# Optimization experiments

Hardware: AMD Instinct MI355X
Metric: run time of the kernel (lower is better)

## Reference

```python
import jax, jax.numpy as jnp
import numpy as np

BETA = 0.25

def conv1d(x, w, b=None, stride=1, pad=0):
    # x: (B, C_in, T), w: (C_out, C_in, K)
    y = jax.lax.conv_general_dilated(x, w, (stride,), [(pad, pad)],
                                     dimension_numbers=('NCW', 'OIW', 'NCW'))
    if b is not None:
        y = y + b[None, :, None]
    return y

def setup_inputs() -> dict:
    key = jax.random.key(0)
    ks = jax.random.split(key, 16)
    B, C_in, T = 64, 64, 4096
    h, rh, D, K = 128, 64, 64, 512
    s = 0.05
    f32 = jnp.float32
    return {
        'x': jax.random.normal(ks[0], (B, C_in, T), f32),
        'w1': jax.random.normal(ks[1], (h // 2, C_in, 4), f32) * s,
        'b1': jnp.zeros((h // 2,), f32),
        'w2': jax.random.normal(ks[2], (h, h // 2, 4), f32) * s,
        'b2': jnp.zeros((h,), f32),
        'w3': jax.random.normal(ks[3], (h, h, 3), f32) * s,
        'b3': jnp.zeros((h,), f32),
        'res0_w1': jax.random.normal(ks[4], (rh, h, 3), f32) * s,
        'res0_w2': jax.random.normal(ks[5], (h, rh, 1), f32) * s,
        'res1_w1': jax.random.normal(ks[6], (rh, h, 3), f32) * s,
        'res1_w2': jax.random.normal(ks[7], (h, rh, 1), f32) * s,
        'w_out': jax.random.normal(ks[8], (D, h, 1), f32) * s,
        'b_out': jnp.zeros((D,), f32),
        'wpq': jax.random.normal(ks[9], (D, D, 1), f32) * s,
        'bpq': jnp.zeros((D,), f32),
        'codebook': jax.random.uniform(ks[10], (K, D), f32, -1.0 / K, 1.0 / K),
    }

def reference(x, w1, b1, w2, b2, w3, b3, res0_w1, res0_w2, res1_w1, res1_w2,
              w_out, b_out, wpq, bpq, codebook):
    # ---- Encoder (1D conv downsampling + residual stack) ----
    hcur = jax.nn.relu(conv1d(x, w1, b1, stride=2, pad=1))       # (B, h/2, T/2)
    hcur = jax.nn.relu(conv1d(hcur, w2, b2, stride=2, pad=1))    # (B, h, T/4)
    hcur = conv1d(hcur, w3, b3, stride=1, pad=1)                 # (B, h, T')
    for wa, wb in ((res0_w1, res0_w2), (res1_w1, res1_w2)):
        hcur = hcur + conv1d(jax.nn.relu(conv1d(jax.nn.relu(hcur), wa, None, 1, 1)), wb, None, 1, 0)
    hcur = jax.nn.relu(hcur)
    hcur = conv1d(hcur, w_out, b_out)                            # (B, D, T')
    # ---- pre-quantization 1x1 conv (module permutes to channel-first and back) ----
    z = conv1d(hcur, wpq, bpq)                                   # (B, D, T')
    z_e = jnp.transpose(z, (0, 2, 1))                            # (B, T', D)
    B, Tq, D = z_e.shape
    K = codebook.shape[0]
    # ---- Vector quantization ----
    flat = z_e.reshape(-1, D)                                    # (N, D)
    d = (jnp.sum(flat * flat, axis=1, keepdims=True)
         + jnp.sum(codebook * codebook, axis=1)[None, :]
         - 2.0 * flat @ codebook.T)                              # (N, K)
    idx = jnp.argmin(d, axis=1)                                  # (N,)
    encodings = jax.nn.one_hot(idx, K, dtype=z_e.dtype)          # (N, K)
    z_q = codebook[idx].reshape(B, Tq, D)                        # gather
    sg = jax.lax.stop_gradient
    embedding_loss = jnp.mean((sg(z_q) - z_e) ** 2) + BETA * jnp.mean((z_q - sg(z_e)) ** 2)
    z_q_st = z_e + sg(z_q - z_e)                                 # straight-through
    e_mean = jnp.mean(encodings, axis=0)
    perplexity = jnp.exp(-jnp.sum(e_mean * jnp.log(e_mean + 1e-10)))
    encoding_indices = idx.reshape(-1, 1)
    return (embedding_loss, z_q_st, perplexity, z_e, encodings, encoding_indices)
```

## Files before the change

### kernel.cpp

```cpp
#include <hip/hip_runtime.h>
#include <math.h>


typedef short short8 __attribute__((ext_vector_type(8)));
typedef float f32x4 __attribute__((ext_vector_type(4)));

__device__ __forceinline__ unsigned short bf16hi(float f) {
  unsigned u = __builtin_bit_cast(unsigned, f);
  return (unsigned short)((u + 0x7FFFu + ((u >> 16) & 1u)) >> 16);
}
__device__ __forceinline__ float bf16tof(unsigned short h) {
  unsigned u = ((unsigned)h) << 16;
  return __builtin_bit_cast(float, u);
}
__device__ __forceinline__ void split3(float f, unsigned short& h,
                                       unsigned short& m, unsigned short& l) {
  h = bf16hi(f);
  float r = f - bf16tof(h);
  m = bf16hi(r);
  l = bf16hi(r - bf16tof(m));
}

template<int CIN, int TAPS, int S, bool RELU_IN, bool HAS_BIAS, bool RESID,
         bool CHW_IN, bool OUT_NOGUARD>
__global__ __launch_bounds__(256) void conv_mfma(
    const float* __restrict__ in, const short* __restrict__ Ab,
    const float* __restrict__ bias, const float* __restrict__ resid,
    float* __restrict__ out, int Tin, int Tout, int MTG)
{
  constexpr int nCk   = CIN / 32;
  constexpr int RS    = (S == 2) ? 130 : ((TAPS == 3) ? 66 : 64);
  constexpr int ROWBS = 40;

  __shared__ short xhi[RS * ROWBS];
  __shared__ short xmd[RS * ROWBS];
  __shared__ short xlo[RS * ROWBS];

  const int tid  = threadIdx.x;
  const int lane = tid & 63;
  const int wv   = tid >> 6;
  const int ih   = wv & 1;
  const int jh   = wv >> 1;
  const int tl   = lane & 15;
  const int q    = lane >> 4;
  const int b    = blockIdx.y;
  const int t0   = blockIdx.x * 64;
  const int co0  = blockIdx.z * 64;
  const int COUT = MTG * 16;

  const int rbase = (S == 2) ? (2 * t0) : ((TAPS == 3) ? t0 : (t0 + 1));

  f32x4 acc[2][2] = {};

  for (int ch = 0; ch < nCk; ch++) {
    if (ch) __syncthreads();

    if constexpr (!CHW_IN) {
      for (int i = tid; i < RS * 8; i += 256) {
        int rl = i >> 3;
        int c4 = (i & 7) * 4;
        int rg = rbase + rl;
        const float* sp = in + ((size_t)b * (Tin + 2) + rg) * CIN + ch * 32 + c4;
        float4 v = *(const float4*)sp;
        if (RELU_IN) {
          v.x = fmaxf(v.x, 0.f); v.y = fmaxf(v.y, 0.f);
          v.z = fmaxf(v.z, 0.f); v.w = fmaxf(v.w, 0.f);
        }
        float vv[4] = {v.x, v.y, v.z, v.w};
        unsigned short h[4], m[4], l[4];
        #pragma unroll
        for (int e = 0; e < 4; e++) split3(vv[e], h[e], m[e], l[e]);
        int slot = (S == 2) ? ((rl & 1) * 65 + (rl >> 1)) : rl;
        int off = slot * ROWBS + c4;
        uint2 uh, um, ul;
        uh.x = (unsigned)h[0] | ((unsigned)h[1] << 16);
        uh.y = (unsigned)h[2] | ((unsigned)h[3] << 16);
        um.x = (unsigned)m[0] | ((unsigned)m[1] << 16);
        um.y = (unsigned)m[2] | ((unsigned)m[3] << 16);
        ul.x = (unsigned)l[0] | ((unsigned)l[1] << 16);
        ul.y = (unsigned)l[2] | ((unsigned)l[3] << 16);
        *(uint2*)(xhi + off) = uh;
        *(uint2*)(xmd + off) = um;
        *(uint2*)(xlo + off) = ul;
      }
    } else {
      if (tid < 32) {
        int cig = ch * 32 + tid;
        int tin = 2 * t0 - 1;
        float v = 0.f;
        if (tin >= 0) v = in[((size_t)b * 64 + cig) * Tin + tin];
        unsigned short h, m, l;
        split3(v, h, m, l);
        xhi[tid] = (short)h;
        xmd[tid] = (short)m;
        xlo[tid] = (short)l;
      }
      int cil = tid >> 3, tq = tid & 7;
      for (int base = tq * 4; base <= 128; base += 32) {
        int tin0 = 2 * t0 + base;
        const float* sp = in + ((size_t)b * 64 + ch * 32 + cil) * Tin + tin0;
        float vv[4];
        if (tin0 + 3 < Tin) {
          float4 t4 = *(const float4*)sp;
          vv[0] = t4.x; vv[1] = t4.y; vv[2] = t4.z; vv[3] = t4.w;
        } else {
          #pragma unroll
          for (int e = 0; e < 4; e++) vv[e] = (tin0 + e < Tin) ? sp[e] : 0.f;
        }
        #pragma unroll
        for (int e = 0; e < 4; e++) {
          int rl = base + e + 1;
          if (rl <= 129) {
            unsigned short h, m, l;
            split3(vv[e], h, m, l);
            int slot = (rl & 1) * 65 + (rl >> 1);
            xhi[slot * ROWBS + cil] = (short)h;
            xmd[slot * ROWBS + cil] = (short)m;
            xlo[slot * ROWBS + cil] = (short)l;
          }
        }
      }
    }
    __syncthreads();

    #pragma unroll
    for (int tap = 0; tap < TAPS; tap++) {
      short8 ah[2], am[2], al[2];
      #pragma unroll
      for (int mi = 0; mi < 2; mi++) {
        const short* ab = Ab +
            (size_t)(((ch * TAPS + tap) * MTG + (co0 >> 4) + ih * 2 + mi) * 3) * 512
            + lane * 8;
        ah[mi] = *(const short8*)ab;
        am[mi] = *(const short8*)(ab + 512);
        al[mi] = *(const short8*)(ab + 1024);
      }
      #pragma unroll
      for (int nt = 0; nt < 2; nt++) {
        int tpos = jh * 32 + nt * 16 + tl;
        int slot;
        if constexpr (S == 2)         slot = (tap & 1) * 65 + tpos + (tap >> 1);
        else if constexpr (TAPS == 3) slot = tpos + tap;
        else                          slot = tpos;
        const int xo = slot * ROWBS + q * 8;
        short8 bh = *(const short8*)(xhi + xo);
        short8 bm = *(const short8*)(xmd + xo);
        short8 bl = *(const short8*)(xlo + xo);
        #pragma unroll
        for (int mi = 0; mi < 2; mi++) {
          acc[mi][nt] = __builtin_amdgcn_mfma_f32_16x16x32_bf16(ah[mi], bh, acc[mi][nt], 0, 0, 0);
          acc[mi][nt] = __builtin_amdgcn_mfma_f32_16x16x32_bf16(ah[mi], bm, acc[mi][nt], 0, 0, 0);
          acc[mi][nt] = __builtin_amdgcn_mfma_f32_16x16x32_bf16(am[mi], bh, acc[mi][nt], 0, 0, 0);
          acc[mi][nt] = __builtin_amdgcn_mfma_f32_16x16x32_bf16(am[mi], bm, acc[mi][nt], 0, 0, 0);
          acc[mi][nt] = __builtin_amdgcn_mfma_f32_16x16x32_bf16(ah[mi], bl, acc[mi][nt], 0, 0, 0);
          acc[mi][nt] = __builtin_amdgcn_mfma_f32_16x16x32_bf16(al[mi], bh, acc[mi][nt], 0, 0, 0);
        }
      }
    }
  }

  #pragma unroll
  for (int mi = 0; mi < 2; mi++) {
    #pragma unroll
    for (int nt = 0; nt < 2; nt++) {
      int t  = t0 + jh * 32 + nt * 16 + tl;
      int co = co0 + (ih * 2 + mi) * 16 + q * 4;
      f32x4 a = acc[mi][nt];
      float4 v = {a[0], a[1], a[2], a[3]};
      if constexpr (HAS_BIAS) {
        float4 bb = *(const float4*)(bias + co);
        v.x += bb.x; v.y += bb.y; v.z += bb.z; v.w += bb.w;
      }
      if constexpr (RESID) {
        float4 rr = *(const float4*)(resid + ((size_t)b * (Tout + 2) + t + 1) * COUT + co);
        v.x += rr.x; v.y += rr.y; v.z += rr.z; v.w += rr.w;
      }
      float* op;
      if constexpr (OUT_NOGUARD) op = out + ((size_t)b * Tout + t) * COUT + co;
      else                       op = out + ((size_t)b * (Tout + 2) + t + 1) * COUT + co;
      *(float4*)op = v;
    }
  }
}

__global__ __launch_bounds__(256) void prep_small(
    const float* __restrict__ wout, const float* __restrict__ bout,
    const float* __restrict__ wpq, const float* __restrict__ bpq,
    const float* __restrict__ cb,
    float* __restrict__ Wc, float* __restrict__ bc, float* __restrict__ cnormd)
{
  const int tid = threadIdx.x;
  for (int i = tid; i < 64 * 128; i += 256) {
    int d = i >> 7, c = i & 127;
    float s = 0.f;
    for (int e = 0; e < 64; e++) s = fmaf(wpq[d * 64 + e], wout[e * 128 + c], s);
    Wc[i] = s;
  }
  for (int i = tid; i < 64; i += 256) {
    float s = bpq[i];
    for (int e = 0; e < 64; e++) s = fmaf(wpq[i * 64 + e], bout[e], s);
    bc[i] = s;
  }
  for (int k = tid; k < 512; k += 256) {
    float s = 0.f;
    for (int d = 0; d < 64; d++) { float c = cb[k * 64 + d]; s = fmaf(c, c, s); }
    cnormd[k] = -0.5f * s;
  }
}

__device__ __forceinline__ void buildA(const float* w, short* dst,
                                       int COUT, int CIN, int TAPS, int idx)
{
  int lane = idx & 63;
  int rest = idx >> 6;
  int hl   = rest % 3;  rest /= 3;
  int mtg  = rest % (COUT / 16); rest /= (COUT / 16);
  int tap  = rest % TAPS;
  int chunk = rest / TAPS;
  int co  = mtg * 16 + (lane & 15);
  int ci0 = chunk * 32 + (lane >> 4) * 8;
  short v[8];
  #pragma unroll
  for (int j = 0; j < 8; j++) {
    float f = w[((size_t)co * CIN + ci0 + j) * TAPS + tap];
    unsigned short h, m, l;
    split3(f, h, m, l);
    v[j] = (hl == 0) ? (short)h : ((hl == 1) ? (short)m : (short)l);
  }
  int MTG = COUT / 16;
  size_t o = ((((size_t)(chunk * TAPS + tap) * MTG + mtg) * 3 + hl) * 64 + lane) * 8;
  #pragma unroll
  for (int j = 0; j < 8; j++) dst[o + j] = v[j];
}

__device__ __forceinline__ void buildAcb(const float* cb, short* dst, int g)
{
  int lane = g & 63;
  int rest = g >> 6;
  int s  = rest % 3; rest /= 3;
  int kc = rest & 1;
  int ct = rest >> 1;
  int tl = lane & 15, q = lane >> 4;
  int code = ct * 16 + tl;
  int k0 = kc * 32 + q * 8;
  size_t o = (((size_t)(ct * 2 + kc) * 3 + s) * 64 + lane) * 8;
  #pragma unroll
  for (int j = 0; j < 8; j++) {
    float f = cb[(size_t)code * 64 + k0 + j];
    unsigned short h, m, l;
    split3(f, h, m, l);
    dst[o + j] = (s == 0) ? (short)h : ((s == 1) ? (short)m : (short)l);
  }
}

__global__ __launch_bounds__(256) void prep_w_all(
    const float* w1, const float* w2, const float* w3,
    const float* r0a, const float* r0b, const float* r1a, const float* r1b,
    const float* Wc, const float* cb,
    short* A1, short* A2, short* A3, short* A4, short* A5, short* A6,
    short* A7, short* A8, short* Acb)
{
  int g = blockIdx.x * 256 + threadIdx.x;
  if      (g < 6144)  buildA(w1,  A1, 64,  64,  4, g);
  else if (g < 18432) buildA(w2,  A2, 128, 64,  4, g - 6144);
  else if (g < 36864) buildA(w3,  A3, 128, 128, 3, g - 18432);
  else if (g < 46080) buildA(r0a, A4, 64,  128, 3, g - 36864);
  else if (g < 49152) buildA(r0b, A5, 128, 64,  1, g - 46080);
  else if (g < 58368) buildA(r1a, A6, 64,  128, 3, g - 49152);
  else if (g < 61440) buildA(r1b, A7, 128, 64,  1, g - 58368);
  else if (g < 64512) buildA(Wc,  A8, 64,  128, 1, g - 61440);
  else if (g < 76800) buildAcb(cb, Acb, g - 64512);
}

__global__ __launch_bounds__(256) void zero_guards(
    float* __restrict__ sA, float* __restrict__ sB1,
    float* __restrict__ sB2, float* __restrict__ sC)
{
  int gt = blockIdx.x * 256 + threadIdx.x;
  int NT = gridDim.x * 256;
  for (int i = gt; i < 64 * 2 * 64; i += NT) {
    int b = i >> 7, r = (i >> 6) & 1, c = i & 63;
    sA[((size_t)b * 2050 + r * 2049) * 64 + c] = 0.f;
  }
  for (int i = gt; i < 64 * 2 * 128; i += NT) {
    int b = i >> 8, r = (i >> 7) & 1, c = i & 127;
    size_t o = ((size_t)b * 1026 + r * 1025) * 128 + c;
    sB1[o] = 0.f; sB2[o] = 0.f;
  }
  for (int i = gt; i < 64 * 2 * 64; i += NT) {
    int b = i >> 7, r = (i >> 6) & 1, c = i & 63;
    sC[((size_t)b * 1026 + r * 1025) * 64 + c] = 0.f;
  }
}

__global__ __launch_bounds__(256) void vq_k(
    const float* __restrict__ ze, const float* __restrict__ cb,
    const float* __restrict__ cnormd, const short* __restrict__ Acb,
    float* __restrict__ zq_out, float* __restrict__ enc,
    float* __restrict__ idx_out,
    int* __restrict__ counts, float* __restrict__ loss_accum)
{
  __shared__ short zh[128 * 72];
  __shared__ short zm[128 * 72];
  __shared__ short zl[128 * 72];
  __shared__ int   idx_s[128];
  __shared__ float ls[4];

  const int tid  = threadIdx.x;
  const int lane = tid & 63;
  const int wv   = tid >> 6;
  const int tl   = lane & 15;
  const int q    = lane >> 4;
  const int n0   = blockIdx.x * 128;

  {
    const float* zb = ze + (size_t)n0 * 64;
    #pragma unroll
    for (int j = 0; j < 8; j++) {
      int off = j * 1024 + tid * 4;
      int p = off >> 6, d = off & 63;
      float2 v0 = *(const float2*)(zb + off);
      float2 v1 = *(const float2*)(zb + off + 2);
      float vv[4] = {v0.x, v0.y, v1.x, v1.y};
      unsigned short h[4], m[4], l[4];
      #pragma unroll
      for (int e = 0; e < 4; e++) split3(vv[e], h[e], m[e], l[e]);
      int o = p * 72 + d;
      uint2 uh, um, ul;
      uh.x = (unsigned)h[0] | ((unsigned)h[1] << 16);
      uh.y = (unsigned)h[2] | ((unsigned)h[3] << 16);
      um.x = (unsigned)m[0] | ((unsigned)m[1] << 16);
      um.y = (unsigned)m[2] | ((unsigned)m[3] << 16);
      ul.x = (unsigned)l[0] | ((unsigned)l[1] << 16);
      ul.y = (unsigned)l[2] | ((unsigned)l[3] << 16);
      *(uint2*)(zh + o) = uh;
      *(uint2*)(zm + o) = um;
      *(uint2*)(zl + o) = ul;
    }
  }
  __syncthreads();

  short8 bh[2][2], bm[2][2], bl[2][2];
  #pragma unroll
  for (int pt = 0; pt < 2; pt++) {
    int row = wv * 32 + pt * 16 + tl;
    #pragma unroll
    for (int kc = 0; kc < 2; kc++) {
      int o = row * 72 + kc * 32 + q * 8;
      bh[pt][kc] = *(const short8*)(zh + o);
      bm[pt][kc] = *(const short8*)(zm + o);
      bl[pt][kc] = *(const short8*)(zl + o);
    }
  }

  float best0 = -3.4e38f, best1 = -3.4e38f;
  int   bi0 = 0, bi1 = 0;

  for (int ct = 0; ct < 32; ct++) {
    float4 cv = *(const float4*)(cnormd + ct * 16 + q * 4);
    f32x4 a0 = {cv.x, cv.y, cv.z, cv.w};
    f32x4 a1 = a0;
    #pragma unroll
    for (int kc = 0; kc < 2; kc++) {
      const short* ap = Acb + (size_t)((ct * 2 + kc) * 3) * 512 + lane * 8;
      short8 ah = *(const short8*)ap;
      short8 am = *(const short8*)(ap + 512);
      short8 al = *(const short8*)(ap + 1024);
      a0 = __builtin_amdgcn_mfma_f32_16x16x32_bf16(ah, bh[0][kc], a0, 0, 0, 0);
      a1 = __builtin_amdgcn_mfma_f32_16x16x32_bf16(ah, bh[1][kc], a1, 0, 0, 0);
      a0 = __builtin_amdgcn_mfma_f32_16x16x32_bf16(ah, bm[0][kc], a0, 0, 0, 0);
      a1 = __builtin_amdgcn_mfma_f32_16x16x32_bf16(ah, bm[1][kc], a1, 0, 0, 0);
      a0 = __builtin_amdgcn_mfma_f32_16x16x32_bf16(am, bh[0][kc], a0, 0, 0, 0);
      a1 = __builtin_amdgcn_mfma_f32_16x16x32_bf16(am, bh[1][kc], a1, 0, 0, 0);
      a0 = __builtin_amdgcn_mfma_f32_16x16x32_bf16(am, bm[0][kc], a0, 0, 0, 0);
      a1 = __builtin_amdgcn_mfma_f32_16x16x32_bf16(am, bm[1][kc], a1, 0, 0, 0);
      a0 = __builtin_amdgcn_mfma_f32_16x16x32_bf16(ah, bl[0][kc], a0, 0, 0, 0);
      a1 = __builtin_amdgcn_mfma_f32_16x16x32_bf16(ah, bl[1][kc], a1, 0, 0, 0);
      a0 = __builtin_amdgcn_mfma_f32_16x16x32_bf16(al, bh[0][kc], a0, 0, 0, 0);
      a1 = __builtin_amdgcn_mfma_f32_16x16x32_bf16(al, bh[1][kc], a1, 0, 0, 0);
    }
    #pragma unroll
    for (int r = 0; r < 4; r++) {
      int code = ct * 16 + q * 4 + r;
      float v0 = a0[r], v1 = a1[r];
      if (v0 > best0) { best0 = v0; bi0 = code; }
      if (v1 > best1) { best1 = v1; bi1 = code; }
    }
  }

  #pragma unroll
  for (int mask = 16; mask <= 32; mask <<= 1) {
    float v0 = __shfl_xor(best0, mask, 64); int i0 = __shfl_xor(bi0, mask, 64);
    float v1 = __shfl_xor(best1, mask, 64); int i1 = __shfl_xor(bi1, mask, 64);
    if (v0 > best0 || (v0 == best0 && i0 < bi0)) { best0 = v0; bi0 = i0; }
    if (v1 > best1 || (v1 == best1 && i1 < bi1)) { best1 = v1; bi1 = i1; }
  }
  if (q == 0) {
    int p0 = wv * 32 + tl;
    int p1 = p0 + 16;
    idx_s[p0] = bi0;
    idx_s[p1] = bi1;
    idx_out[n0 + p0] = (float)bi0;
    idx_out[n0 + p1] = (float)bi1;
    atomicAdd(&counts[bi0], 1);
    atomicAdd(&counts[bi1], 1);
  }
  __syncthreads();

  float lsum = 0.f;
  const size_t obase = (size_t)n0 * 64;
  #pragma unroll
  for (int j = 0; j < 32; j++) {
    int pos = j * 256 + tid;
    int p = pos >> 6, d = pos & 63;
    int id = idx_s[p];
    float zq  = cb[id * 64 + d];
    float zev = ze[obase + pos];
    float df  = zq - zev;
    lsum = fmaf(df, df, lsum);
    zq_out[obase + pos] = zq;
  }
  #pragma unroll
  for (int off = 32; off; off >>= 1) lsum += __shfl_down(lsum, off, 64);
  if (lane == 0) ls[wv] = lsum;

  for (int pp = 0; pp < 128; pp += 2) {
    int p   = pp + (tid >> 7);
    int col = (tid & 127) * 4;
    int id  = idx_s[p];
    float4 v;
    v.x = (col     == id) ? 1.0f : 0.0f;
    v.y = (col + 1 == id) ? 1.0f : 0.0f;
    v.z = (col + 2 == id) ? 1.0f : 0.0f;
    v.w = (col + 3 == id) ? 1.0f : 0.0f;
    *(float4*)(enc + (size_t)(n0 + p) * 512 + col) = v;
  }

  __syncthreads();
  if (tid == 0) atomicAdd(loss_accum, ls[0] + ls[1] + ls[2] + ls[3]);
}

__global__ __launch_bounds__(256) void fin_k(
    const int* __restrict__ counts, const float* __restrict__ loss_accum,
    float* __restrict__ loss_out, float* __restrict__ perp_out)
{
  __shared__ float sd[256];
  const int tid = threadIdx.x;
  float h = 0.f;
  for (int k = tid; k < 512; k += 256) {
    float em = (float)counts[k] * (1.0f / 65536.0f);
    h += em * logf(em + 1e-10f);
  }
  sd[tid] = h;
  __syncthreads();
  for (int s = 128; s; s >>= 1) {
    if (tid < s) sd[tid] += sd[tid + s];
    __syncthreads();
  }
  if (tid == 0) {
    *perp_out = expf(-sd[0]);
    *loss_out = *loss_accum * 1.25f / 4194304.f;
  }
}

extern "C" void kernel_launch(void* const* d_in, const int* in_sizes, int n_in,
                              void* d_out, int out_size, void* d_ws, size_t ws_size,
                              hipStream_t stream)
{
  const float* x    = (const float*)d_in[0];
  const float* w1   = (const float*)d_in[1];
  const float* b1   = (const float*)d_in[2];
  const float* w2   = (const float*)d_in[3];
  const float* b2   = (const float*)d_in[4];
  const float* w3   = (const float*)d_in[5];
  const float* b3   = (const float*)d_in[6];
  const float* r0a  = (const float*)d_in[7];
  const float* r0b  = (const float*)d_in[8];
  const float* r1a  = (const float*)d_in[9];
  const float* r1b  = (const float*)d_in[10];
  const float* wout = (const float*)d_in[11];
  const float* bout = (const float*)d_in[12];
  const float* wpq  = (const float*)d_in[13];
  const float* bpq  = (const float*)d_in[14];
  const float* cb   = (const float*)d_in[15];

  float* out = (float*)d_out;
  float* f   = (float*)d_ws;

  float* slotA  = f;
  float* slotB1 = f + 8396800;
  float* slotB2 = f + 16801792;
  float* slotC  = f + 25206784;
  float* Wcf    = f + 29409280;
  float* bc     = f + 29417472;
  float* cnormd = f + 29417536;
  int*   counts = (int*)(f + 29418048);
  float* lossa  = f + 29418560;
  short* AB     = (short*)(f + 29418576);
  short* A1 = AB;
  short* A2 = AB + 49152;
  short* A3 = AB + 147456;
  short* A4 = AB + 294912;
  short* A5 = AB + 368640;
  short* A6 = AB + 393216;
  short* A7 = AB + 466944;
  short* A8 = AB + 491520;
  short* Acb = (short*)(f + 29676624);

  float* loss_out = out;
  float* zq_out   = out + 1;
  float* perp_out = out + 4194305;
  float* ze_out   = out + 4194306;
  float* enc_out  = out + 8388610;
  float* idx_out  = out + 41943042;

  prep_small<<<dim3(1), dim3(256), 0, stream>>>(wout, bout, wpq, bpq, cb,
                                                Wcf, bc, cnormd);
  prep_w_all<<<dim3(300), dim3(256), 0, stream>>>(w1, w2, w3, r0a, r0b, r1a,
                                                  r1b, Wcf, cb,
                                                  A1, A2, A3, A4, A5, A6, A7,
                                                  A8, Acb);
  zero_guards<<<dim3(32), dim3(256), 0, stream>>>(slotA, slotB1, slotB2, slotC);
  hipMemsetAsync(counts, 0, 2052, stream);

  conv_mfma<64, 4, 2, false, true, false, true, false>
      <<<dim3(32, 64, 1), dim3(256), 0, stream>>>(x, A1, b1, nullptr, slotA,
                                                  4096, 2048, 4);
  conv_mfma<64, 4, 2, true, true, false, false, false>
      <<<dim3(16, 64, 2), dim3(256), 0, stream>>>(slotA, A2, b2, nullptr, slotB1,
                                                  2048, 1024, 8);
  conv_mfma<128, 3, 1, true, true, false, false, false>
      <<<dim3(16, 64, 2), dim3(256), 0, stream>>>(slotB1, A3, b3, nullptr, slotB2,
                                                  1024, 1024, 8);
  conv_mfma<128, 3, 1, true, false, false, false, false>
      <<<dim3(16, 64, 1), dim3(256), 0, stream>>>(slotB2, A4, nullptr, nullptr,
                                                  slotC, 1024, 1024, 4);
  conv_mfma<64, 1, 1, true, false, true, false, false>
      <<<dim3(16, 64, 2), dim3(256), 0, stream>>>(slotC, A5, nullptr, slotB2,
                                                  slotB1, 1024, 1024, 8);
  conv_mfma<128, 3, 1, true, false, false, false, false>
      <<<dim3(16, 64, 1), dim3(256), 0, stream>>>(slotB1, A6, nullptr, nullptr,
                                                  slotC, 1024, 1024, 4);
  conv_mfma<64, 1, 1, true, false, true, false, false>
      <<<dim3(16, 64, 2), dim3(256), 0, stream>>>(slotC, A7, nullptr, slotB1,
                                                  slotB2, 1024, 1024, 8);
  conv_mfma<128, 1, 1, true, true, false, false, true>
      <<<dim3(16, 64, 1), dim3(256), 0, stream>>>(slotB2, A8, bc, nullptr,
                                                  ze_out, 1024, 1024, 4);

  vq_k<<<dim3(512), dim3(256), 0, stream>>>(ze_out, cb, cnormd, Acb, zq_out,
                                            enc_out, idx_out, counts, lossa);
  fin_k<<<dim3(1), dim3(256), 0, stream>>>(counts, lossa, loss_out, perp_out);
}
```

Measured before the change: 698.2 us.

## Split VQ into argmax kernel and wide-grid output writer with nontemporal stores

The fused VQ kernel is split in two. The first kernel computes the argmin indices and counts and writes the indices to a scratch buffer. A second kernel with 4096 blocks gathers codebook rows, accumulates the loss, and writes z_q and the 128 MB one-hot encodings using vectorized nontemporal stores. The aim is to spread the store-bound output writes over many more blocks and keep them from polluting the cache. The cost is an extra launch and an index round-trip through global memory.

```diff
diff --git a/kernel.cpp b/kernel.cpp
--- a/kernel.cpp
+++ b/kernel.cpp
@@ -19,6 +19,11 @@
   float r = f - bf16tof(h);
   m = bf16hi(r);
   l = bf16hi(r - bf16tof(m));
+}
+__device__ __forceinline__ void nt_store4(float* p, float a, float b,
+                                          float c, float d) {
+  f32x4 v = {a, b, c, d};
+  __builtin_nontemporal_store(v, (f32x4*)p);
 }
 
 template<int CIN, int TAPS, int S, bool RELU_IN, bool HAS_BIAS, bool RESID,
@@ -293,18 +298,15 @@
   }
 }
 
-__global__ __launch_bounds__(256) void vq_k(
-    const float* __restrict__ ze, const float* __restrict__ cb,
-    const float* __restrict__ cnormd, const short* __restrict__ Acb,
-    float* __restrict__ zq_out, float* __restrict__ enc,
-    float* __restrict__ idx_out,
-    int* __restrict__ counts, float* __restrict__ loss_accum)
+__global__ __launch_bounds__(256) void vq_argmax(
+    const float* __restrict__ ze, const float* __restrict__ cnormd,
+    const short* __restrict__ Acb,
+    float* __restrict__ idx_out, int* __restrict__ idxw,
+    int* __restrict__ counts)
 {
   __shared__ short zh[128 * 72];
   __shared__ short zm[128 * 72];
   __shared__ short zl[128 * 72];
-  __shared__ int   idx_s[128];
-  __shared__ float ls[4];
 
   const int tid  = threadIdx.x;
   const int lane = tid & 63;
@@ -398,42 +400,55 @@
   if (q == 0) {
     int p0 = wv * 32 + tl;
     int p1 = p0 + 16;
-    idx_s[p0] = bi0;
-    idx_s[p1] = bi1;
     idx_out[n0 + p0] = (float)bi0;
     idx_out[n0 + p1] = (float)bi1;
+    idxw[n0 + p0] = bi0;
+    idxw[n0 + p1] = bi1;
     atomicAdd(&counts[bi0], 1);
     atomicAdd(&counts[bi1], 1);
   }
+}
+
+__global__ __launch_bounds__(256) void vq_write(
+    const float* __restrict__ ze, const float* __restrict__ cb,
+    const int* __restrict__ idxw,
+    float* __restrict__ zq_out, float* __restrict__ enc,
+    float* __restrict__ loss_accum)
+{
+  __shared__ int   ids[16];
+  __shared__ float ls[4];
+  const int tid = threadIdx.x;
+  const int n0  = blockIdx.x * 16;
+
+  if (tid < 16) ids[tid] = idxw[n0 + tid];
   __syncthreads();
 
-  float lsum = 0.f;
-  const size_t obase = (size_t)n0 * 64;
-  #pragma unroll
-  for (int j = 0; j < 32; j++) {
-    int pos = j * 256 + tid;
-    int p = pos >> 6, d = pos & 63;
-    int id = idx_s[p];
-    float zq  = cb[id * 64 + d];
-    float zev = ze[obase + pos];
-    float df  = zq - zev;
-    lsum = fmaf(df, df, lsum);
-    zq_out[obase + pos] = zq;
-  }
+  const int p  = tid >> 4;
+  const int d0 = (tid & 15) * 4;
+  const int id = ids[p];
+  float4 c4 = *(const float4*)(cb + (size_t)id * 64 + d0);
+  const size_t zoff = (size_t)(n0 + p) * 64 + d0;
+  float4 z4 = *(const float4*)(ze + zoff);
+  float dx = c4.x - z4.x, dy = c4.y - z4.y;
+  float dz = c4.z - z4.z, dw = c4.w - z4.w;
+  float lsum = fmaf(dx, dx, fmaf(dy, dy, fmaf(dz, dz, dw * dw)));
+  nt_store4(zq_out + zoff, c4.x, c4.y, c4.z, c4.w);
+
   #pragma unroll
   for (int off = 32; off; off >>= 1) lsum += __shfl_down(lsum, off, 64);
-  if (lane == 0) ls[wv] = lsum;
-
-  for (int pp = 0; pp < 128; pp += 2) {
-    int p   = pp + (tid >> 7);
-    int col = (tid & 127) * 4;
-    int id  = idx_s[p];
-    float4 v;
-    v.x = (col     == id) ? 1.0f : 0.0f;
-    v.y = (col + 1 == id) ? 1.0f : 0.0f;
-    v.z = (col + 2 == id) ? 1.0f : 0.0f;
-    v.w = (col + 3 == id) ? 1.0f : 0.0f;
-    *(float4*)(enc + (size_t)(n0 + p) * 512 + col) = v;
+  if ((tid & 63) == 0) ls[tid >> 6] = lsum;
+
+  #pragma unroll
+  for (int k = 0; k < 8; k++) {
+    int i = k * 256 + tid;
+    int r = i >> 7;
+    int c = (i & 127) * 4;
+    int idr = ids[r];
+    nt_store4(enc + (size_t)(n0 + r) * 512 + c,
+              (c     == idr) ? 1.0f : 0.0f,
+              (c + 1 == idr) ? 1.0f : 0.0f,
+              (c + 2 == idr) ? 1.0f : 0.0f,
+              (c + 3 == idr) ? 1.0f : 0.0f);
   }
 
   __syncthreads();
@@ -506,6 +521,7 @@
   short* A7 = AB + 466944;
   short* A8 = AB + 491520;
   short* Acb = (short*)(f + 29676624);
+  int*   idxw = (int*)(f + 29725776);
 
   float* loss_out = out;
   float* zq_out   = out + 1;
@@ -548,7 +564,9 @@
       <<<dim3(16, 64, 1), dim3(256), 0, stream>>>(slotB2, A8, bc, nullptr,
                                                   ze_out, 1024, 1024, 4);
 
-  vq_k<<<dim3(512), dim3(256), 0, stream>>>(ze_out, cb, cnormd, Acb, zq_out,
-                                            enc_out, idx_out, counts, lossa);
+  vq_argmax<<<dim3(512), dim3(256), 0, stream>>>(ze_out, cnormd, Acb,
+                                                 idx_out, idxw, counts);
+  vq_write<<<dim3(4096), dim3(256), 0, stream>>>(ze_out, cb, idxw,
+                                                 zq_out, enc_out, lossa);
   fin_k<<<dim3(1), dim3(256), 0, stream>>>(counts, lossa, loss_out, perp_out);
 }
```

Measured after the change: 704.9 us. No clear change (+1.0%).
